# Performance work log

Hardware: AMD Instinct MI355X
Metric: run time of the kernel (lower is better)

The kernel has to match this reference:

```python
import jax, jax.numpy as jnp
import numpy as np

SCALE = 64.0  # quantization scale: float -> signed 8-bit index
PAD = 1
K = 3


def setup_inputs() -> dict:
    key = jax.random.key(0)
    k1, k2, k3 = jax.random.split(key, 3)
    x = jax.random.normal(k1, (8, 64, 32, 32), dtype=jnp.float32)
    weight = jax.random.normal(k2, (64, 64, 3, 3), dtype=jnp.float32) * 0.1
    bias = jax.random.normal(k3, (64,), dtype=jnp.float32)
    # 256x256 approximate-multiplier LUT: dequantized exact product perturbed by a
    # deterministic relative error, emulating an MBM approximate multiplier table.
    q = (np.arange(256, dtype=np.float64) - 128.0) / SCALE
    exact = np.outer(q, q)
    rng = np.random.default_rng(0)
    lut = (exact * (1.0 + 0.02 * rng.standard_normal((256, 256)))).astype(np.float32)
    return {"x": x, "weight": weight, "bias": bias, "lut": jnp.asarray(lut)}


def reference(x, weight, bias, lut):
    B, C, H, W = x.shape
    O = weight.shape[0]
    oh = (H + 2 * PAD - K) + 1
    ow = (W + 2 * PAD - K) + 1
    L = oh * ow
    P = C * K * K

    xp = jnp.pad(x, ((0, 0), (0, 0), (PAD, PAD), (PAD, PAD)))
    # im2col: [B, C*K*K, oh, ow], feature dim ordered channel-slowest (matches
    # torch unfold(2,k).unfold(3,k).reshape ordering intent)
    patches = jax.lax.conv_general_dilated_patches(xp, (K, K), (1, 1), 'VALID')
    patches = patches.reshape(B, P, L)

    # quantize both operands to 8-bit LUT indices in [0, 255]
    qx = jnp.clip(jnp.round(patches * SCALE), -128, 127).astype(jnp.int32) + 128  # [B,P,L]
    qw = jnp.clip(jnp.round(weight.reshape(O, P) * SCALE), -128, 127).astype(jnp.int32) + 128  # [O,P]

    lut_flat = lut.reshape(-1)
    base = qx * 256  # row offsets, loop-invariant  [B,P,L]

    def body(carry, wrow):  # wrow: [P] indices for one output channel
        prod = jnp.take(lut_flat, base + wrow[None, :, None], axis=0)  # [B,P,L]
        return carry, prod.sum(axis=1)  # [B,L]

    _, out = jax.lax.scan(body, 0.0, qw)  # [O,B,L]
    out = out.transpose(1, 0, 2).reshape(B, O, oh, ow)
    return out + bias[None, :, None, None]
```

## Files before the change

kernel.cpp:

```cpp
#include <hip/hip_runtime.h>
#include <hip/hip_fp16.h>


#define NT 256

__device__ __forceinline__ int quantize(float v) {
    int q = (int)rintf(v * 64.0f);
    q = q < -128 ? -128 : q;
    q = q > 127 ? 127 : q;
    return q + 128;
}

__device__ __forceinline__ void gll16(const void* g, void* l) {
    __builtin_amdgcn_global_load_lds(
        (const __attribute__((address_space(1))) unsigned int*)g,
        (__attribute__((address_space(3))) unsigned int*)l, 16, 0, 0);
}

__global__ __launch_bounds__(NT, 2)
void build_T3(const float* __restrict__ w, const float* __restrict__ lut,
              unsigned int* __restrict__ T)
{
    __shared__ float band[16 * 257];
    __shared__ unsigned char qw2[2][576];

    const int tid = threadIdx.x;
    const int pair = blockIdx.x >> 4;
    const int qq = (blockIdx.x & 15) << 4;

    for (int i = tid; i < 1152; i += NT) {
        int os = i >= 576;
        int idx = i - os * 576;
        qw2[os][idx] = (unsigned char)quantize(w[(pair * 2 + os) * 576 + idx]);
    }
    for (int i = tid; i < 16 * 256; i += NT) {
        int r = i >> 8, c2 = i & 255;
        band[r * 257 + c2] = lut[(qq + r) * 256 + c2];
    }
    __syncthreads();

    for (int it = 0; it < 12; ++it) {
        int idx = it * NT + tid;
        int c = idx / 48;
        int rem = idx - c * 48;
        int ky = rem >> 4;
        int qxl = rem & 15;
        const float* brow = band + qxl * 257;
        const unsigned char* q0 = &qw2[0][c * 9 + ky * 3];
        const unsigned char* q1 = &qw2[1][c * 9 + ky * 3];
        unsigned int wd[3];
        #pragma unroll
        for (int k = 0; k < 3; ++k) {
            unsigned int h0 = __half_as_ushort(__float2half(brow[q0[k]]));
            unsigned int h1 = __half_as_ushort(__float2half(brow[q1[k]]));
            wd[k] = h0 | (h1 << 16);
        }
        unsigned int* dst = T + ((size_t)((pair * 64 + c) * 3 + ky) * 256 + qq + qxl) * 3;
        dst[0] = wd[0]; dst[1] = wd[1]; dst[2] = wd[2];
    }
}

__global__ __launch_bounds__(NT, 2)
void approx_main(const float* __restrict__ x, const unsigned int* __restrict__ T,
                 const float* __restrict__ bias, float* __restrict__ out)
{
    __shared__ __align__(16) unsigned char Ts[36864];
    __shared__ unsigned int plane[4][2][180];

    const int tid = threadIdx.x;
    const int bid = blockIdx.x;
    const int pair = bid & 31;
    const int bh = bid >> 5;
    const int b = bh >> 1;
    const int h = bh & 1;

    const int parity = tid >> 6;
    const int lt = tid & 63;
    const int yl = lt >> 2;
    const int xs = lt & 3;
    const int x0 = xs << 3;
    const int yg = (h << 4) + yl;

    const char* Tg = (const char*)T + (size_t)pair * 589824;
    const float* xb = x + (size_t)b * 65536;

    const int halo_g  = h ? 15 : 16;
    const int halo_pr = h ? 0  : 17;

    for (int i = tid; i < 1440; i += NT) ((unsigned int*)plane)[i] = 0x80808080u;

    float4 xv0 = *(const float4*)(xb + parity * 1024 + yg * 32 + x0);
    float4 xv1 = *(const float4*)(xb + parity * 1024 + yg * 32 + x0 + 4);
    float xh = (lt < 32) ? xb[parity * 1024 + halo_g * 32 + lt] : 0.f;

    __syncthreads();

    const __half2 z2 = __float2half2_rn(0.f);
    float a32[8], b32[8];
    __half2 acc2[8];
    #pragma unroll
    for (int k = 0; k < 8; ++k) { a32[k] = 0.f; b32[k] = 0.f; acc2[k] = z2; }

    for (int t = 0; t < 16; ++t) {
        const int buf = t & 1;
        unsigned char* pb = (unsigned char*)plane[parity][buf];
        unsigned int pk0 = (unsigned int)quantize(xv0.x) |
                           ((unsigned int)quantize(xv0.y) << 8) |
                           ((unsigned int)quantize(xv0.z) << 16) |
                           ((unsigned int)quantize(xv0.w) << 24);
        unsigned int pk1 = (unsigned int)quantize(xv1.x) |
                           ((unsigned int)quantize(xv1.y) << 8) |
                           ((unsigned int)quantize(xv1.z) << 16) |
                           ((unsigned int)quantize(xv1.w) << 24);
        *(unsigned int*)(pb + (yl + 1) * 40 + 4 + x0)     = pk0;
        *(unsigned int*)(pb + (yl + 1) * 40 + 4 + x0 + 4) = pk1;
        if (lt < 32) pb[halo_pr * 40 + 4 + lt] = (unsigned char)quantize(xh);

        {
            const char* src = Tg + t * 36864 + tid * 16;
            char* dst = (char*)Ts + tid * 16;
            #pragma unroll
            for (int k = 0; k < 9; ++k) gll16(src + k * 4096, dst + k * 4096);
        }
        if (t < 15) {
            const int c1 = 4 * (t + 1) + parity;
            xv0 = *(const float4*)(xb + c1 * 1024 + yg * 32 + x0);
            xv1 = *(const float4*)(xb + c1 * 1024 + yg * 32 + x0 + 4);
            if (lt < 32) xh = xb[c1 * 1024 + halo_g * 32 + lt];
        }
        __syncthreads();

        const unsigned int* pl = plane[parity][buf];
        const char* Tc = (const char*)Ts + parity * 9216;
        #pragma unroll
        for (int ky = 0; ky < 3; ++ky) {
            const int prow = (yl + ky) * 10 + (x0 >> 2);
            uint2 ua = *(const uint2*)&pl[prow];
            uint2 ub = *(const uint2*)&pl[prow + 2];
            int m[10];
            m[0] = (int)(ua.x >> 24);
            m[1] = (int)(ua.y & 255u);  m[2] = (int)((ua.y >> 8) & 255u);
            m[3] = (int)((ua.y >> 16) & 255u); m[4] = (int)(ua.y >> 24);
            m[5] = (int)(ub.x & 255u);  m[6] = (int)((ub.x >> 8) & 255u);
            m[7] = (int)((ub.x >> 16) & 255u); m[8] = (int)(ub.x >> 24);
            m[9] = (int)(ub.y & 255u);
            const char* Tk = Tc + ky * 3072;
            #pragma unroll
            for (int j = 0; j < 10; ++j) {
                const unsigned int* R = (const unsigned int*)(Tk + m[j] * 12);
                if (j <= 7) {
                    unsigned int w0 = R[0];
                    acc2[j] = __hadd2(acc2[j], *(const __half2*)&w0);
                }
                if (j >= 1 && j <= 8) {
                    unsigned int w1 = R[1];
                    acc2[j - 1] = __hadd2(acc2[j - 1], *(const __half2*)&w1);
                }
                if (j >= 2) {
                    unsigned int w2 = R[2];
                    acc2[j - 2] = __hadd2(acc2[j - 2], *(const __half2*)&w2);
                }
            }
        }
        if (t & 1) {
            #pragma unroll
            for (int k = 0; k < 8; ++k) {
                a32[k] += __low2float(acc2[k]);
                b32[k] += __high2float(acc2[k]);
                acc2[k] = z2;
            }
        }
        __syncthreads();
    }

    float* red = (float*)Ts;
    if (parity) {
        #pragma unroll
        for (int k = 0; k < 8; ++k) {
            red[(parity - 1) * 1024 + lt * 16 + k]     = a32[k];
            red[(parity - 1) * 1024 + lt * 16 + 8 + k] = b32[k];
        }
    }
    __syncthreads();
    if (!parity) {
        const int o0 = pair * 2;
        float bo0 = bias[o0], bo1 = bias[o0 + 1];
        float r0[8], r1[8];
        #pragma unroll
        for (int k = 0; k < 8; ++k) {
            r0[k] = a32[k] + red[lt * 16 + k] + red[1024 + lt * 16 + k]
                  + red[2048 + lt * 16 + k] + bo0;
            r1[k] = b32[k] + red[lt * 16 + 8 + k] + red[1024 + lt * 16 + 8 + k]
                  + red[2048 + lt * 16 + 8 + k] + bo1;
        }
        float* p0 = out + ((size_t)b * 64 + o0) * 1024 + yg * 32 + x0;
        *(float4*)(p0)     = make_float4(r0[0], r0[1], r0[2], r0[3]);
        *(float4*)(p0 + 4) = make_float4(r0[4], r0[5], r0[6], r0[7]);
        float* p1 = p0 + 1024;
        *(float4*)(p1)     = make_float4(r1[0], r1[1], r1[2], r1[3]);
        *(float4*)(p1 + 4) = make_float4(r1[4], r1[5], r1[6], r1[7]);
    }
}

#define BW1 61
__global__ __launch_bounds__(NT, 2)
void approxconv2d_v1(const float* __restrict__ x,
                     const float* __restrict__ w,
                     const float* __restrict__ bias,
                     const float* __restrict__ lut,
                     float* __restrict__ out)
{
    __shared__ float band[256 * BW1];
    __shared__ unsigned int plane[340];
    __shared__ unsigned char qwrow[576];
    __shared__ int s_min;

    const int tid = threadIdx.x;
    const int bid = blockIdx.x;
    const int b = bid >> 6;
    const int o = bid & 63;

    if (tid == 0) s_min = 255;
    for (int i = tid; i < 340; i += NT) plane[i] = 0x80808080u;
    __syncthreads();

    int lmin = 255;
    for (int i = tid; i < 576; i += NT) {
        int q = quantize(w[o * 576 + i]);
        qwrow[i] = (unsigned char)q;
        lmin = lmin < q ? lmin : q;
    }
    atomicMin(&s_min, lmin);
    __syncthreads();

    int cmin = s_min;
    if (cmin > 256 - BW1) cmin = 256 - BW1;

    for (int i = tid; i < 256 * BW1; i += NT) {
        int qx = i / BW1;
        int cc = i - qx * BW1;
        band[i] = lut[(qx << 8) + cmin + cc];
    }

    const int y  = tid >> 3;
    const int xq = tid & 7;
    const int x0 = xq << 2;

    float acc0 = 0.f, acc1 = 0.f, acc2 = 0.f, acc3 = 0.f;
    const float* xb = x + (size_t)b * 64 * 1024;
    unsigned char* pb = (unsigned char*)plane;

    for (int c = 0; c < 64; ++c) {
        __syncthreads();
        float4 xv = *(const float4*)(xb + c * 1024 + y * 32 + x0);
        int qa = quantize(xv.x), qb = quantize(xv.y);
        int qc = quantize(xv.z), qd = quantize(xv.w);
        int wbase = (y + 1) * 40 + x0 + 1;
        pb[wbase + 0] = (unsigned char)qa;
        pb[wbase + 1] = (unsigned char)qb;
        pb[wbase + 2] = (unsigned char)qc;
        pb[wbase + 3] = (unsigned char)qd;
        __syncthreads();

        const unsigned char* qwp = qwrow + c * 9;
        #pragma unroll
        for (int ky = 0; ky < 3; ++ky) {
            int ro = (y + ky) * 10 + xq;
            unsigned int r0 = plane[ro];
            unsigned int r1 = plane[ro + 1];
            int ee[6];
            ee[0] = (int)(r0 & 255u);
            ee[1] = (int)((r0 >> 8) & 255u);
            ee[2] = (int)((r0 >> 16) & 255u);
            ee[3] = (int)(r0 >> 24);
            ee[4] = (int)(r1 & 255u);
            ee[5] = (int)((r1 >> 8) & 255u);
            int pp[6];
            #pragma unroll
            for (int tt = 0; tt < 6; ++tt) pp[tt] = ee[tt] * BW1;
            #pragma unroll
            for (int kx = 0; kx < 3; ++kx) {
                int cq = (int)qwp[ky * 3 + kx];
                int cc = cq - cmin;
                if ((unsigned)cc < (unsigned)BW1) {
                    acc0 += band[pp[kx + 0] + cc];
                    acc1 += band[pp[kx + 1] + cc];
                    acc2 += band[pp[kx + 2] + cc];
                    acc3 += band[pp[kx + 3] + cc];
                } else {
                    acc0 += lut[(ee[kx + 0] << 8) + cq];
                    acc1 += lut[(ee[kx + 1] << 8) + cq];
                    acc2 += lut[(ee[kx + 2] << 8) + cq];
                    acc3 += lut[(ee[kx + 3] << 8) + cq];
                }
            }
        }
    }

    float bo = bias[o];
    float4 r;
    r.x = acc0 + bo; r.y = acc1 + bo; r.z = acc2 + bo; r.w = acc3 + bo;
    *(float4*)(out + (size_t)bid * 1024 + y * 32 + x0) = r;
}

extern "C" void kernel_launch(void* const* d_in, const int* in_sizes, int n_in,
                              void* d_out, int out_size, void* d_ws, size_t ws_size,
                              hipStream_t stream) {
    const float* x    = (const float*)d_in[0];
    const float* wgt  = (const float*)d_in[1];
    const float* bias = (const float*)d_in[2];
    const float* lut  = (const float*)d_in[3];
    float* out = (float*)d_out;

    const size_t T_BYTES = (size_t)32 * 64 * 3 * 256 * 12;
    if (ws_size >= T_BYTES) {
        hipLaunchKernelGGL(build_T3, dim3(512), dim3(NT), 0, stream,
                           wgt, lut, (unsigned int*)d_ws);
        hipLaunchKernelGGL(approx_main, dim3(512), dim3(NT), 0, stream,
                           x, (const unsigned int*)d_ws, bias, out);
    } else {
        hipLaunchKernelGGL(approxconv2d_v1, dim3(512), dim3(NT), 0, stream,
                           x, wgt, bias, lut, out);
    }
}
```

Baseline: 53.96 us.

## Split work into quarter-image tiles with four pixels per thread and 1024 blocks

The main kernel now tiles each image into four 8-row strips with four pixels per thread instead of two 16-row halves with eight. This doubles the block count and raises the occupancy hint from 2 to 4 blocks per SM. The table-building kernel is also split into 1024 blocks with smaller LUT bands. The cost is that each block loads the same per-channel T slice into LDS for half the output work, doubling T traffic and halo overhead, in exchange for more parallelism across the GPU's CUs.

```diff
diff --git a/kernel.cpp b/kernel.cpp
--- a/kernel.cpp
+++ b/kernel.cpp
@@ -21,112 +21,105 @@
 void build_T3(const float* __restrict__ w, const float* __restrict__ lut,
               unsigned int* __restrict__ T)
 {
-    __shared__ float band[16 * 257];
+    __shared__ float band[8 * 257];
     __shared__ unsigned char qw2[2][576];
 
     const int tid = threadIdx.x;
-    const int pair = blockIdx.x >> 4;
-    const int qq = (blockIdx.x & 15) << 4;
+    const int pair = blockIdx.x >> 5;
+    const int qq = (blockIdx.x & 31) << 3;
 
     for (int i = tid; i < 1152; i += NT) {
         int os = i >= 576;
         int idx = i - os * 576;
         qw2[os][idx] = (unsigned char)quantize(w[(pair * 2 + os) * 576 + idx]);
     }
-    for (int i = tid; i < 16 * 256; i += NT) {
+    for (int i = tid; i < 8 * 256; i += NT) {
         int r = i >> 8, c2 = i & 255;
         band[r * 257 + c2] = lut[(qq + r) * 256 + c2];
     }
     __syncthreads();
 
-    for (int it = 0; it < 12; ++it) {
+    for (int it = 0; it < 6; ++it) {
         int idx = it * NT + tid;
-        int c = idx / 48;
-        int rem = idx - c * 48;
-        int ky = rem >> 4;
-        int qxl = rem & 15;
+        int c = idx / 24;
+        int rem = idx - c * 24;
+        int ky = rem >> 3;
+        int qxl = rem & 7;
         const float* brow = band + qxl * 257;
         const unsigned char* q0 = &qw2[0][c * 9 + ky * 3];
         const unsigned char* q1 = &qw2[1][c * 9 + ky * 3];
-        unsigned int wd[3];
+        unsigned int* dst =
+            T + ((size_t)((pair * 64 + c) * 3 + ky) * 256 + qq + qxl) * 3;
         #pragma unroll
         for (int k = 0; k < 3; ++k) {
             unsigned int h0 = __half_as_ushort(__float2half(brow[q0[k]]));
             unsigned int h1 = __half_as_ushort(__float2half(brow[q1[k]]));
-            wd[k] = h0 | (h1 << 16);
-        }
-        unsigned int* dst = T + ((size_t)((pair * 64 + c) * 3 + ky) * 256 + qq + qxl) * 3;
-        dst[0] = wd[0]; dst[1] = wd[1]; dst[2] = wd[2];
-    }
-}
-
-__global__ __launch_bounds__(NT, 2)
+            dst[k] = h0 | (h1 << 16);
+        }
+    }
+}
+
+__global__ __launch_bounds__(NT, 4)
 void approx_main(const float* __restrict__ x, const unsigned int* __restrict__ T,
                  const float* __restrict__ bias, float* __restrict__ out)
 {
     __shared__ __align__(16) unsigned char Ts[36864];
-    __shared__ unsigned int plane[4][2][180];
+    __shared__ unsigned int plane[4][2][100];
 
     const int tid = threadIdx.x;
     const int bid = blockIdx.x;
     const int pair = bid & 31;
-    const int bh = bid >> 5;
-    const int b = bh >> 1;
-    const int h = bh & 1;
+    const int g = bid >> 5;
+    const int b = g >> 2;
+    const int qt = g & 3;
 
     const int parity = tid >> 6;
     const int lt = tid & 63;
-    const int yl = lt >> 2;
-    const int xs = lt & 3;
-    const int x0 = xs << 3;
-    const int yg = (h << 4) + yl;
+    const int yl = lt >> 3;
+    const int x0 = (lt & 7) << 2;
+    const int yg = qt * 8 + yl;
 
     const char* Tg = (const char*)T + (size_t)pair * 589824;
     const float* xb = x + (size_t)b * 65536;
 
-    const int halo_g  = h ? 15 : 16;
-    const int halo_pr = h ? 0  : 17;
-
-    for (int i = tid; i < 1440; i += NT) ((unsigned int*)plane)[i] = 0x80808080u;
-
-    float4 xv0 = *(const float4*)(xb + parity * 1024 + yg * 32 + x0);
-    float4 xv1 = *(const float4*)(xb + parity * 1024 + yg * 32 + x0 + 4);
-    float xh = (lt < 32) ? xb[parity * 1024 + halo_g * 32 + lt] : 0.f;
+    for (int i = tid; i < 800; i += NT) ((unsigned int*)plane)[i] = 0x80808080u;
+
+    const int hr = lt >> 5;
+    const int hcol = lt & 31;
+    const int hgrow = qt * 8 + (hr ? 8 : -1);
+    const int hvalid = (hgrow >= 0 && hgrow < 32);
+    const int hpr = hr ? 9 : 0;
+
+    float4 xv = *(const float4*)(xb + parity * 1024 + yg * 32 + x0);
+    float xh = hvalid ? xb[parity * 1024 + hgrow * 32 + hcol] : 0.f;
 
     __syncthreads();
 
     const __half2 z2 = __float2half2_rn(0.f);
-    float a32[8], b32[8];
-    __half2 acc2[8];
-    #pragma unroll
-    for (int k = 0; k < 8; ++k) { a32[k] = 0.f; b32[k] = 0.f; acc2[k] = z2; }
+    __half2 acc2[4] = {z2, z2, z2, z2};
+    float a0[4] = {0.f, 0.f, 0.f, 0.f};
+    float a1[4] = {0.f, 0.f, 0.f, 0.f};
 
     for (int t = 0; t < 16; ++t) {
         const int buf = t & 1;
         unsigned char* pb = (unsigned char*)plane[parity][buf];
-        unsigned int pk0 = (unsigned int)quantize(xv0.x) |
-                           ((unsigned int)quantize(xv0.y) << 8) |
-                           ((unsigned int)quantize(xv0.z) << 16) |
-                           ((unsigned int)quantize(xv0.w) << 24);
-        unsigned int pk1 = (unsigned int)quantize(xv1.x) |
-                           ((unsigned int)quantize(xv1.y) << 8) |
-                           ((unsigned int)quantize(xv1.z) << 16) |
-                           ((unsigned int)quantize(xv1.w) << 24);
-        *(unsigned int*)(pb + (yl + 1) * 40 + 4 + x0)     = pk0;
-        *(unsigned int*)(pb + (yl + 1) * 40 + 4 + x0 + 4) = pk1;
-        if (lt < 32) pb[halo_pr * 40 + 4 + lt] = (unsigned char)quantize(xh);
+        unsigned int pk = (unsigned int)quantize(xv.x) |
+                          ((unsigned int)quantize(xv.y) << 8) |
+                          ((unsigned int)quantize(xv.z) << 16) |
+                          ((unsigned int)quantize(xv.w) << 24);
+        *(unsigned int*)(pb + (yl + 1) * 40 + 4 + x0) = pk;
+        if (hvalid) pb[hpr * 40 + 4 + hcol] = (unsigned char)quantize(xh);
 
         {
-            const char* src = Tg + t * 36864 + tid * 16;
+            const char* src = Tg + (size_t)t * 36864 + tid * 16;
             char* dst = (char*)Ts + tid * 16;
             #pragma unroll
             for (int k = 0; k < 9; ++k) gll16(src + k * 4096, dst + k * 4096);
         }
         if (t < 15) {
-            const int c1 = 4 * (t + 1) + parity;
-            xv0 = *(const float4*)(xb + c1 * 1024 + yg * 32 + x0);
-            xv1 = *(const float4*)(xb + c1 * 1024 + yg * 32 + x0 + 4);
-            if (lt < 32) xh = xb[c1 * 1024 + halo_g * 32 + lt];
+            const int cn = 4 * (t + 1) + parity;
+            xv = *(const float4*)(xb + cn * 1024 + yg * 32 + x0);
+            if (hvalid) xh = xb[cn * 1024 + hgrow * 32 + hcol];
         }
         __syncthreads();
 
@@ -134,40 +127,39 @@
         const char* Tc = (const char*)Ts + parity * 9216;
         #pragma unroll
         for (int ky = 0; ky < 3; ++ky) {
-            const int prow = (yl + ky) * 10 + (x0 >> 2);
-            uint2 ua = *(const uint2*)&pl[prow];
-            uint2 ub = *(const uint2*)&pl[prow + 2];
-            int m[10];
-            m[0] = (int)(ua.x >> 24);
-            m[1] = (int)(ua.y & 255u);  m[2] = (int)((ua.y >> 8) & 255u);
-            m[3] = (int)((ua.y >> 16) & 255u); m[4] = (int)(ua.y >> 24);
-            m[5] = (int)(ub.x & 255u);  m[6] = (int)((ub.x >> 8) & 255u);
-            m[7] = (int)((ub.x >> 16) & 255u); m[8] = (int)(ub.x >> 24);
-            m[9] = (int)(ub.y & 255u);
-            const char* Tk = Tc + ky * 3072;
-            #pragma unroll
-            for (int j = 0; j < 10; ++j) {
-                const unsigned int* R = (const unsigned int*)(Tk + m[j] * 12);
-                if (j <= 7) {
-                    unsigned int w0 = R[0];
-                    acc2[j] = __hadd2(acc2[j], *(const __half2*)&w0);
-                }
-                if (j >= 1 && j <= 8) {
-                    unsigned int w1 = R[1];
-                    acc2[j - 1] = __hadd2(acc2[j - 1], *(const __half2*)&w1);
-                }
-                if (j >= 2) {
-                    unsigned int w2 = R[2];
-                    acc2[j - 2] = __hadd2(acc2[j - 2], *(const __half2*)&w2);
-                }
-            }
+            const int w0 = (yl + ky) * 10 + (x0 >> 2);
+            uint2 ua = *(const uint2*)&pl[w0];
+            unsigned int uc = pl[w0 + 2];
+            int m0 = (int)(ua.x >> 24);
+            int m1 = (int)(ua.y & 255u), m2 = (int)((ua.y >> 8) & 255u);
+            int m3 = (int)((ua.y >> 16) & 255u), m4 = (int)(ua.y >> 24);
+            int m5 = (int)(uc & 255u);
+            const unsigned int* Tk = (const unsigned int*)(Tc + ky * 3072);
+            const unsigned int* R0 = Tk + m0 * 3;
+            acc2[0] = __hadd2(acc2[0], *(const __half2*)&R0[0]);
+            const unsigned int* R1 = Tk + m1 * 3;
+            acc2[1] = __hadd2(acc2[1], *(const __half2*)&R1[0]);
+            acc2[0] = __hadd2(acc2[0], *(const __half2*)&R1[1]);
+            const unsigned int* R2 = Tk + m2 * 3;
+            acc2[2] = __hadd2(acc2[2], *(const __half2*)&R2[0]);
+            acc2[1] = __hadd2(acc2[1], *(const __half2*)&R2[1]);
+            acc2[0] = __hadd2(acc2[0], *(const __half2*)&R2[2]);
+            const unsigned int* R3 = Tk + m3 * 3;
+            acc2[3] = __hadd2(acc2[3], *(const __half2*)&R3[0]);
+            acc2[2] = __hadd2(acc2[2], *(const __half2*)&R3[1]);
+            acc2[1] = __hadd2(acc2[1], *(const __half2*)&R3[2]);
+            const unsigned int* R4 = Tk + m4 * 3;
+            acc2[3] = __hadd2(acc2[3], *(const __half2*)&R4[1]);
+            acc2[2] = __hadd2(acc2[2], *(const __half2*)&R4[2]);
+            const unsigned int* R5 = Tk + m5 * 3;
+            acc2[3] = __hadd2(acc2[3], *(const __half2*)&R5[2]);
         }
         if (t & 1) {
             #pragma unroll
-            for (int k = 0; k < 8; ++k) {
-                a32[k] += __low2float(acc2[k]);
-                b32[k] += __high2float(acc2[k]);
-                acc2[k] = z2;
+            for (int p2 = 0; p2 < 4; ++p2) {
+                a0[p2] += __low2float(acc2[p2]);
+                a1[p2] += __high2float(acc2[p2]);
+                acc2[p2] = z2;
             }
         }
         __syncthreads();
@@ -176,29 +168,26 @@
     float* red = (float*)Ts;
     if (parity) {
         #pragma unroll
-        for (int k = 0; k < 8; ++k) {
-            red[(parity - 1) * 1024 + lt * 16 + k]     = a32[k];
-            red[(parity - 1) * 1024 + lt * 16 + 8 + k] = b32[k];
+        for (int p2 = 0; p2 < 4; ++p2) {
+            red[(parity - 1) * 512 + lt * 8 + p2]     = a0[p2];
+            red[(parity - 1) * 512 + lt * 8 + 4 + p2] = a1[p2];
         }
     }
     __syncthreads();
     if (!parity) {
         const int o0 = pair * 2;
         float bo0 = bias[o0], bo1 = bias[o0 + 1];
-        float r0[8], r1[8];
-        #pragma unroll
-        for (int k = 0; k < 8; ++k) {
-            r0[k] = a32[k] + red[lt * 16 + k] + red[1024 + lt * 16 + k]
-                  + red[2048 + lt * 16 + k] + bo0;
-            r1[k] = b32[k] + red[lt * 16 + 8 + k] + red[1024 + lt * 16 + 8 + k]
-                  + red[2048 + lt * 16 + 8 + k] + bo1;
-        }
-        float* p0 = out + ((size_t)b * 64 + o0) * 1024 + yg * 32 + x0;
-        *(float4*)(p0)     = make_float4(r0[0], r0[1], r0[2], r0[3]);
-        *(float4*)(p0 + 4) = make_float4(r0[4], r0[5], r0[6], r0[7]);
-        float* p1 = p0 + 1024;
-        *(float4*)(p1)     = make_float4(r1[0], r1[1], r1[2], r1[3]);
-        *(float4*)(p1 + 4) = make_float4(r1[4], r1[5], r1[6], r1[7]);
+        float4 r0, r1;
+        float* q0 = &r0.x; float* q1 = &r1.x;
+        #pragma unroll
+        for (int p2 = 0; p2 < 4; ++p2) {
+            q0[p2] = a0[p2] + red[lt * 8 + p2] + red[512 + lt * 8 + p2]
+                   + red[1024 + lt * 8 + p2] + bo0;
+            q1[p2] = a1[p2] + red[lt * 8 + 4 + p2] + red[512 + lt * 8 + 4 + p2]
+                   + red[1024 + lt * 8 + 4 + p2] + bo1;
+        }
+        *(float4*)(out + ((size_t)b * 64 + o0) * 1024 + yg * 32 + x0) = r0;
+        *(float4*)(out + ((size_t)b * 64 + o0 + 1) * 1024 + yg * 32 + x0) = r1;
     }
 }
 
@@ -314,9 +303,9 @@
 
     const size_t T_BYTES = (size_t)32 * 64 * 3 * 256 * 12;
     if (ws_size >= T_BYTES) {
-        hipLaunchKernelGGL(build_T3, dim3(512), dim3(NT), 0, stream,
+        hipLaunchKernelGGL(build_T3, dim3(1024), dim3(NT), 0, stream,
                            wgt, lut, (unsigned int*)d_ws);
-        hipLaunchKernelGGL(approx_main, dim3(512), dim3(NT), 0, stream,
+        hipLaunchKernelGGL(approx_main, dim3(1024), dim3(NT), 0, stream,
                            x, (const unsigned int*)d_ws, bias, out);
     } else {
         hipLaunchKernelGGL(approxconv2d_v1, dim3(512), dim3(NT), 0, stream,
```

Result: slower. 75.09 us (+39.2%).
